# Kernel tuning notes

Measured on AMD Instinct MI355X. Metric: run time of the kernel, lower is better.

The kernel has to match this reference:

```python
import jax, jax.numpy as jnp
import numpy as np

D = 256            # number of graph nodes (example.size(3))
K1 = D // 2        # topkpool1 k
K2 = D // 4        # topkpool2 k
B = 8


def _lrelu(x):
    return jnp.where(x > 0, x, 0.33 * x)


def _e2e(h, wa, ba, wb, bb):
    # h: [B,C,d,d]; wa,wb: [P,C,d] (squeezed (1,d)/(d,1) conv kernels)
    # cnn1: contract over columns j -> [B,P,d]; cnn2: contract over rows i -> [B,P,d]
    a = jnp.einsum('bcij,pcj->bpi', h, wa) + ba[None, :, None]
    b = jnp.einsum('bcij,pci->bpj', h, wb) + bb[None, :, None]
    # cat([a]*d, 3) + cat([b]*d, 2)  ==  broadcast-add
    return a[:, :, :, None] + b[:, :, None, :]


def _gcn(h, g, W, b):
    # h: [B,N,F_in], g: [B,N,N]; faithful to norm_g: g[i,j] / deg[j] (column-normalized
    # because torch broadcasts the [N] degree vector over the LAST dim)
    gb = (g > 0).astype(h.dtype)
    deg = gb.sum(axis=2)                      # [B,N] row sums
    gn = gb / deg[:, None, :]                 # divide column j by deg[j]
    return jnp.einsum('bij,bjf->bif', gn, h) @ W.T + b


def _pool(h, g, s, k):
    # h: [B,N,F], g: [B,N,N], s: [B,N,1] -> top-k nodes by score (descending)
    vals, idx = jax.lax.top_k(s[:, :, 0], k)              # [B,k]
    hn = jnp.take_along_axis(h, idx[:, :, None], axis=1)  # [B,k,F]
    gn = jnp.take_along_axis(g, idx[:, :, None], axis=1)
    gn = jnp.take_along_axis(gn, idx[:, None, :], axis=2) # [B,k,k]
    return hn, gn, vals[:, :, None]


def _readout(h):
    # h: [B,N,F] (node axis = 1); torch ReadOut on [B,F,N,1] max/mean over dim=2
    return jnp.concatenate([h.max(axis=1), h.mean(axis=1)], axis=1)  # [B,2F]


def _forward(x, w1a, b1a, w1b, b1b, w2a, b2a, w2b, b2b, e2n_w, e2n_b,
             a11_w, a11_b, a12_w, a12_b, g1_w, g1_b,
             a21_w, a21_b, a22_w, a22_b,
             d1_w, d1_b, d2_w, d2_b, d3_w, d3_b):
    h = _lrelu(_e2e(x, w1a, b1a, w1b, b1b))         # [B,128,d,d]
    h = _lrelu(_e2e(h, w2a, b2a, w2b, b2b))         # [B,256,d,d]
    # E2N conv (1,d): [B,8,d,1] -> node features [B,d,8]
    nodes = _lrelu(jnp.einsum('bcij,pcj->bpi', h, e2n_w) + e2n_b[None, :, None])
    nodes = jnp.transpose(nodes, (0, 2, 1))          # [B,d,8]
    g0 = x[:, 0]                                     # [B,d,d]

    w = _lrelu(_gcn(nodes, g0, a11_w, a11_b))        # [B,d,1]
    w = jax.nn.sigmoid(_gcn(w, g0, a12_w, a12_b))
    h1, g1, s1 = _pool(nodes, g0, w, K1)             # [B,K1,8], [B,K1,K1], [B,K1,1]
    out = h1 * s1 + h1
    sum1 = _readout(out)                             # [B,16]

    h2 = _gcn(out, g1, g1_w, g1_b)                   # [B,K1,8] (no activation, as in torch)
    w = _lrelu(_gcn(h2, g1, a21_w, a21_b))
    w = jax.nn.sigmoid(_gcn(w, g1, a22_w, a22_b))
    h3, g2, s2 = _pool(h2, g1, w, K2)                # [B,K2,8]
    out2 = h3 * s2 + h3
    sum2 = _readout(out2)                            # [B,16]

    z = sum1 + sum2                                  # [B,16]
    z = _lrelu(z @ d1_w.T + d1_b)                    # dropout = identity (eval mode)
    z = _lrelu(z @ d2_w.T + d2_b)
    return z @ d3_w.T + d3_b                         # [B,1]


def setup_inputs() -> dict:
    key = jax.random.key(0)
    ks = jax.random.split(key, 16)
    f32 = jnp.float32

    def rn(k, shape, scale):
        return jax.random.normal(k, shape, dtype=f32) * scale

    return {
        'x': jax.random.normal(ks[0], (B, 1, D, D), dtype=f32),
        'w1a': rn(ks[1], (128, 1, D), 0.08),  'b1a': jnp.zeros((128,), f32),
        'w1b': rn(ks[2], (128, 1, D), 0.08),  'b1b': jnp.zeros((128,), f32),
        'w2a': rn(ks[3], (256, 128, D), 0.008), 'b2a': jnp.zeros((256,), f32),
        'w2b': rn(ks[4], (256, 128, D), 0.008), 'b2b': jnp.zeros((256,), f32),
        'e2n_w': rn(ks[5], (8, 256, D), 0.005), 'e2n_b': jnp.zeros((8,), f32),
        'a11_w': rn(ks[6], (1, 8), 0.3),  'a11_b': jnp.zeros((1,), f32),
        'a12_w': rn(ks[7], (1, 1), 0.3),  'a12_b': jnp.zeros((1,), f32),
        'g1_w': rn(ks[8], (8, 8), 0.3),   'g1_b': jnp.zeros((8,), f32),
        'a21_w': rn(ks[9], (1, 8), 0.3),  'a21_b': jnp.zeros((1,), f32),
        'a22_w': rn(ks[10], (1, 1), 0.3), 'a22_b': jnp.zeros((1,), f32),
        'd1_w': rn(ks[11], (128, 16), 0.2), 'd1_b': jnp.zeros((128,), f32),
        'd2_w': rn(ks[12], (64, 128), 0.08), 'd2_b': jnp.zeros((64,), f32),
        'd3_w': rn(ks[13], (1, 64), 0.1),  'd3_b': jnp.zeros((1,), f32),
    }


def reference(x, w1a, b1a, w1b, b1b, w2a, b2a, w2b, b2b, e2n_w, e2n_b,
              a11_w, a11_b, a12_w, a12_b, g1_w, g1_b,
              a21_w, a21_b, a22_w, a22_b,
              d1_w, d1_b, d2_w, d2_b, d3_w, d3_b):
    return _forward(x, w1a, b1a, w1b, b1b, w2a, b2a, w2b, b2b, e2n_w, e2n_b,
                    a11_w, a11_b, a12_w, a12_b, g1_w, g1_b,
                    a21_w, a21_b, a22_w, a22_b,
                    d1_w, d1_b, d2_w, d2_b, d3_w, d3_b)
```

## Files before the change

### kernel.cpp

```cpp
#include <hip/hip_runtime.h>

typedef short s16x8 __attribute__((ext_vector_type(8)));
typedef float f32x4 __attribute__((ext_vector_type(4)));
typedef float f32x2 __attribute__((ext_vector_type(2)));

#define TID threadIdx.x

__device__ __forceinline__ float lrelu_f(float x) { return fmaxf(x, 0.33f * x); }

__device__ __forceinline__ unsigned lrelu_pack(float pv, f32x2 q) {
    f32x2 s = q + pv;
    f32x2 m = s * 0.33f;
    f32x2 r = __builtin_elementwise_max(s, m);
    unsigned u;
    asm("v_cvt_pk_bf16_f32 %0, %1, %2" : "=v"(u) : "v"(r.x), "v"(r.y));
    return u;
}
__device__ __forceinline__ unsigned pk_bf16(float a, float b) {
    unsigned u;
    asm("v_cvt_pk_bf16_f32 %0, %1, %2" : "=v"(u) : "v"(a), "v"(b));
    return u;
}

union FragU { s16x8 v; uint4 q; unsigned w[4]; };

__global__ __launch_bounds__(256) void k_convert(
    const float* __restrict__ sa, unsigned short* __restrict__ da, int na4,
    const float* __restrict__ sb, unsigned short* __restrict__ db, int nb4,
    const float* __restrict__ sc, unsigned short* __restrict__ dc, int nc4)
{
    const float* s; unsigned short* d; int n4;
    if (blockIdx.y == 0)      { s = sa; d = da; n4 = na4; }
    else if (blockIdx.y == 1) { s = sb; d = db; n4 = nb4; }
    else                      { s = sc; d = dc; n4 = nc4; }
    const int stride = gridDim.x * 256;
    for (int i = blockIdx.x * 256 + TID; i < n4; i += stride) {
        float4 v = ((const float4*)s)[i];
        ((uint2*)d)[i] = make_uint2(pk_bf16(v.x, v.y), pk_bf16(v.z, v.w));
    }
}

__global__ __launch_bounds__(128) void k_l1(
    const float* __restrict__ x,
    const float* __restrict__ w1a, const float* __restrict__ b1a,
    const float* __restrict__ w1b, const float* __restrict__ b1b,
    float* __restrict__ A1, float* __restrict__ B1)
{
    const int r = blockIdx.x, b = blockIdx.y, v = blockIdx.z;
    const int tid = TID;
    __shared__ float xr[256];
    const float* xb = x + b * 65536;
    if (v == 0) {
        xr[tid]       = xb[r * 256 + tid];
        xr[tid + 128] = xb[r * 256 + tid + 128];
    } else {
        xr[tid]       = xb[tid * 256 + r];
        xr[tid + 128] = xb[(tid + 128) * 256 + r];
    }
    __syncthreads();
    const float* w    = v ? w1b : w1a;
    const float* bias = v ? b1b : b1a;
    float* OUT = v ? B1 : A1;
    float acc = bias[tid];
    const float* wr = w + tid * 256;
    #pragma unroll 4
    for (int q = 0; q < 256; q += 8) {
        float4 a = *(const float4*)(wr + q);
        float4 c = *(const float4*)(wr + q + 4);
        acc += xr[q + 0] * a.x + xr[q + 1] * a.y + xr[q + 2] * a.z + xr[q + 3] * a.w;
        acc += xr[q + 4] * c.x + xr[q + 5] * c.y + xr[q + 6] * c.z + xr[q + 7] * c.w;
    }
    OUT[b * 32768 + tid * 256 + r] = acc;
}

__global__ __launch_bounds__(512) void k_e2e(
    const float* __restrict__ A1, const float* __restrict__ B1,
    const unsigned short* __restrict__ w2aM, const unsigned short* __restrict__ w2bM,
    float* __restrict__ part)
{
    const int rt = blockIdx.x;
    const int s  = blockIdx.y;
    const int bw = blockIdx.z;
    const int b = bw >> 1, which = bw & 1;
    const float* P = (which ? B1 : A1) + b * 32768;
    const float* Q = (which ? A1 : B1) + b * 32768;
    const unsigned short* W = which ? w2bM : w2aM;
    const int c0 = s * 16, r0 = rt * 128;

    __shared__ float Qs[16][256];
    __shared__ float Ps[16][128];

    const int tid = TID;
    {
        const float4* Qg = (const float4*)(Q + c0 * 256);
        float4* Qd = (float4*)&Qs[0][0];
        Qd[tid]       = Qg[tid];
        Qd[tid + 512] = Qg[tid + 512];
        int row = tid >> 5, col = tid & 31;
        *(float4*)&Ps[row][col * 4] = *(const float4*)&P[(c0 + row) * 256 + r0 + col * 4];
    }
    __syncthreads();

    const int wave = tid >> 6, lane = tid & 63, quad = lane >> 4, l16 = lane & 15;
    const int wi = wave & 3, wj = wave >> 2;
    const int pbase = wi * 64, rbase = wj * 64;

    f32x4 acc[4][4] = {};

    const unsigned short* Wrow[4];
    #pragma unroll
    for (int pf = 0; pf < 4; ++pf)
        Wrow[pf] = W + (size_t)(pbase + pf * 16 + l16) * 32768 + c0 * 256 + quad * 8;

    FragU af[2][4];
    f32x2 qp[2][4];
    float pv[4], pvn[4];

    #pragma unroll
    for (int pf = 0; pf < 4; ++pf) af[0][pf].q = *(const uint4*)(Wrow[pf]);
    #pragma unroll
    for (int k = 0; k < 4; ++k) qp[0][k] = *(const f32x2*)&Qs[0][quad * 8 + 2 * k];
    #pragma unroll
    for (int nf = 0; nf < 4; ++nf) pv[nf] = Ps[0][rbase + nf * 16 + l16];

    for (int c = 0; c < 16; ++c) {
        #pragma unroll
        for (int q0 = 0; q0 < 8; ++q0) {
            const int cur = q0 & 1, nxt = cur ^ 1;
            const int cn = (q0 == 7) ? c + 1 : c;
            const int qn = (q0 + 1) & 7;
            if (cn < 16) {
                #pragma unroll
                for (int pf = 0; pf < 4; ++pf)
                    af[nxt][pf].q = *(const uint4*)(Wrow[pf] + cn * 256 + qn * 32);
                #pragma unroll
                for (int k = 0; k < 4; ++k)
                    qp[nxt][k] = *(const f32x2*)&Qs[cn][qn * 32 + quad * 8 + 2 * k];
            }
            if (q0 == 4 && c + 1 < 16) {
                #pragma unroll
                for (int nf = 0; nf < 4; ++nf) pvn[nf] = Ps[c + 1][rbase + nf * 16 + l16];
            }
            #pragma unroll
            for (int nf = 0; nf < 4; ++nf) {
                FragU hb;
                hb.w[0] = lrelu_pack(pv[nf], qp[cur][0]);
                hb.w[1] = lrelu_pack(pv[nf], qp[cur][1]);
                hb.w[2] = lrelu_pack(pv[nf], qp[cur][2]);
                hb.w[3] = lrelu_pack(pv[nf], qp[cur][3]);
                #pragma unroll
                for (int pf = 0; pf < 4; ++pf)
                    acc[pf][nf] = __builtin_amdgcn_mfma_f32_16x16x32_bf16(af[cur][pf].v, hb.v, acc[pf][nf], 0, 0, 0);
            }
            if (q0 == 7) {
                #pragma unroll
                for (int nf = 0; nf < 4; ++nf) pv[nf] = pvn[nf];
            }
        }
    }
    float* pb = part + (size_t)(s * 16 + bw) * 65536;
    #pragma unroll
    for (int pf = 0; pf < 4; ++pf)
        #pragma unroll
        for (int nf = 0; nf < 4; ++nf)
            #pragma unroll
            for (int t = 0; t < 4; ++t) {
                int p = pbase + pf * 16 + quad * 4 + t;
                int r = r0 + rbase + nf * 16 + l16;
                pb[p * 256 + r] = acc[pf][nf][t];
            }
}

__global__ __launch_bounds__(256) void k_red(
    const float* __restrict__ part,
    const float* __restrict__ b2a, const float* __restrict__ b2b,
    float* __restrict__ A2, float* __restrict__ B2)
{
    const int bw = blockIdx.y; const int b = bw >> 1, which = bw & 1;
    const int idx = blockIdx.x * 256 + TID;
    const float4* pp = (const float4*)part;
    float4 acc = make_float4(0.f, 0.f, 0.f, 0.f);
    #pragma unroll
    for (int s = 0; s < 8; ++s) {
        float4 v = pp[(size_t)(s * 16 + bw) * 16384 + idx];
        acc.x += v.x; acc.y += v.y; acc.z += v.z; acc.w += v.w;
    }
    const int p = idx >> 6;
    const float bias = (which ? b2b : b2a)[p];
    acc.x += bias; acc.y += bias; acc.z += bias; acc.w += bias;
    float* OUT = (which ? B2 : A2) + b * 65536;
    ((float4*)OUT)[idx] = acc;
}

__global__ __launch_bounds__(256) void k_e2n(
    const float* __restrict__ A2, const float* __restrict__ B2,
    const unsigned short* __restrict__ e2nw,
    float* __restrict__ nodes_raw)
{
    const int it = blockIdx.x, b = blockIdx.y, sn = blockIdx.z;
    const int tid = TID, wave = tid >> 6, lane = tid & 63, quad = lane >> 4, l16 = lane & 15;
    const int i0 = it * 16;
    const int c0 = sn * 32 + wave * 8;
    const float* Ab = A2 + b * 65536;
    const float* Bb = B2 + b * 65536;
    const float* Brow0 = Bb + c0 * 256 + quad * 8;
    const unsigned short* Wrow0 = e2nw + (size_t)l16 * 65536 + c0 * 256 + quad * 8;

    f32x4 acc = {};
    FragU af[2];
    f32x2 qp[2][4];
    float pv, pvn;

    if (l16 < 8) af[0].q = *(const uint4*)(Wrow0);
    else         af[0].q = make_uint4(0u, 0u, 0u, 0u);
    #pragma unroll
    for (int k = 0; k < 4; ++k) qp[0][k] = *(const f32x2*)(Brow0 + 2 * k);
    pv = Ab[c0 * 256 + i0 + l16];

    for (int cc = 0; cc < 8; ++cc) {
        #pragma unroll
        for (int q0 = 0; q0 < 8; ++q0) {
            const int cur = q0 & 1, nxt = cur ^ 1;
            const int cn = (q0 == 7) ? cc + 1 : cc;
            const int qn = (q0 + 1) & 7;
            if (cn < 8) {
                if (l16 < 8) af[nxt].q = *(const uint4*)(Wrow0 + cn * 256 + qn * 32);
                else         af[nxt].q = make_uint4(0u, 0u, 0u, 0u);
                #pragma unroll
                for (int k = 0; k < 4; ++k)
                    qp[nxt][k] = *(const f32x2*)(Brow0 + cn * 256 + qn * 32 + 2 * k);
            }
            if (q0 == 4 && cc + 1 < 8) pvn = Ab[(c0 + cc + 1) * 256 + i0 + l16];
            FragU hb;
            hb.w[0] = lrelu_pack(pv, qp[cur][0]);
            hb.w[1] = lrelu_pack(pv, qp[cur][1]);
            hb.w[2] = lrelu_pack(pv, qp[cur][2]);
            hb.w[3] = lrelu_pack(pv, qp[cur][3]);
            acc = __builtin_amdgcn_mfma_f32_16x16x32_bf16(af[cur].v, hb.v, acc, 0, 0, 0);
            if (q0 == 7) pv = pvn;
        }
    }
    __shared__ float red[4][16][16];
    #pragma unroll
    for (int t = 0; t < 4; ++t) red[wave][quad * 4 + t][l16] = acc[t];
    __syncthreads();
    const int row = tid >> 4, col = tid & 15;
    if (row < 8) {
        float ssum = red[0][row][col] + red[1][row][col] + red[2][row][col] + red[3][row][col];
        atomicAdd(&nodes_raw[b * 2048 + (i0 + col) * 8 + row], ssum);
    }
}

__global__ __launch_bounds__(256) void k_adj(
    const float* __restrict__ x,
    unsigned long long* __restrict__ adjw, float* __restrict__ rdegw)
{
    const int b = blockIdx.y;
    const int tid = TID, wave = tid >> 6, lane = tid & 63;
    const int rbase = blockIdx.x * 32 + wave * 8;
    for (int rr = 0; rr < 8; ++rr) {
        const int row = rbase + rr;
        int d = 0;
        unsigned long long w[4];
        #pragma unroll
        for (int k = 0; k < 4; ++k) {
            float v = x[b * 65536 + row * 256 + k * 64 + lane];
            w[k] = __ballot(v > 0.0f);
            d += __popcll(w[k]);
        }
        if (lane == 0) {
            #pragma unroll
            for (int k = 0; k < 4; ++k) adjw[(b * 256 + row) * 4 + k] = w[k];
            rdegw[b * 256 + row] = d ? 1.0f / (float)d : 0.0f;
        }
    }
}

__global__ __launch_bounds__(256) void k_tail(
    const unsigned long long* __restrict__ adjw, const float* __restrict__ rdegw,
    const float* __restrict__ nodes_raw, const float* __restrict__ e2n_b,
    const float* __restrict__ a11_w, const float* __restrict__ a11_b,
    const float* __restrict__ a12_w, const float* __restrict__ a12_b,
    const float* __restrict__ g1_w,  const float* __restrict__ g1_b,
    const float* __restrict__ a21_w, const float* __restrict__ a21_b,
    const float* __restrict__ a22_w, const float* __restrict__ a22_b,
    const float* __restrict__ d1_w,  const float* __restrict__ d1_b,
    const float* __restrict__ d2_w,  const float* __restrict__ d2_b,
    const float* __restrict__ d3_w,  const float* __restrict__ d3_b,
    float* __restrict__ out)
{
    const int b = blockIdx.x;
    const int tid = TID;

    __shared__ unsigned long long adj[256][4];
    __shared__ float nod[256][8];
    __shared__ float rdeg[256];
    __shared__ float md[256];
    __shared__ float w1s[256];
    __shared__ float w2s[256];
    __shared__ int   selflag[256];
    __shared__ int   selidx[128];
    __shared__ float s1v[128];
    __shared__ float out1[128][8];
    __shared__ float aggL[128][8];
    __shared__ float h2L[128][8];
    __shared__ unsigned long long adj1[128][2];
    __shared__ float rdeg1[128];
    __shared__ float tA[128];
    __shared__ float w1t[128];
    __shared__ float w2t[128];
    __shared__ int   sel2flag[128];
    __shared__ int   sel2idx[64];
    __shared__ float s2v[64];
    __shared__ float out2[64][8];
    __shared__ float r1[16], r2[16], zz[16];
    __shared__ float z1[128];
    __shared__ float z2[64];

    if (tid < 128) { selidx[tid] = 0; s1v[tid] = 0.0f; }
    if (tid < 64)  { sel2idx[tid] = 0; s2v[tid] = 0.0f; }

    {
        #pragma unroll
        for (int k = 0; k < 4; ++k) adj[tid][k] = adjw[(b * 256 + tid) * 4 + k];
        rdeg[tid] = rdegw[b * 256 + tid];
        for (int f = 0; f < 8; ++f)
            nod[tid][f] = lrelu_f(nodes_raw[b * 2048 + tid * 8 + f] + e2n_b[f]);
    }
    __syncthreads();
    {
        float s = 0.0f;
        for (int f = 0; f < 8; ++f) s += nod[tid][f] * a11_w[f];
        md[tid] = s * rdeg[tid];
    }
    __syncthreads();
    {
        float s = 0.0f;
        for (int k = 0; k < 4; ++k) {
            unsigned long long m = adj[tid][k];
            while (m) { int j = __builtin_ctzll(m); m &= m - 1; s += md[k * 64 + j]; }
        }
        w1s[tid] = lrelu_f(s + a11_b[0]);
    }
    __syncthreads();
    md[tid] = w1s[tid] * a12_w[0] * rdeg[tid];
    __syncthreads();
    {
        float s = 0.0f;
        for (int k = 0; k < 4; ++k) {
            unsigned long long m = adj[tid][k];
            while (m) { int j = __builtin_ctzll(m); m &= m - 1; s += md[k * 64 + j]; }
        }
        w2s[tid] = 1.0f / (1.0f + expf(-(s + a12_b[0])));
    }
    __syncthreads();
    {
        const float my = w2s[tid];
        int cnt = 0;
        for (int j = 0; j < 256; ++j) {
            float o = w2s[j];
            cnt += (o > my) || (o == my && j < tid);
        }
        selflag[tid] = (cnt < 128) ? 1 : 0;
    }
    __syncthreads();
    if (selflag[tid]) {
        int pos = 0;
        for (int j = 0; j < tid; ++j) pos += selflag[j];
        if (pos < 128) { selidx[pos] = tid; s1v[pos] = w2s[tid]; }
    }
    __syncthreads();
    for (int k = tid; k < 1024; k += 256) {
        int t = k >> 3, f = k & 7;
        out1[t][f] = nod[selidx[t]][f] * (1.0f + s1v[t]);
    }
    __syncthreads();
    if (tid < 16) {
        int f = tid & 7;
        if (tid < 8) {
            float mx = -INFINITY;
            for (int t = 0; t < 128; ++t) mx = fmaxf(mx, out1[t][f]);
            r1[tid] = mx;
        } else {
            float s = 0.0f;
            for (int t = 0; t < 128; ++t) s += out1[t][f];
            r1[tid] = s * (1.0f / 128.0f);
        }
    }
    if (tid < 128) {
        unsigned long long wds[2] = {0ull, 0ull};
        const int gi = selidx[tid];
        for (int u = 0; u < 128; ++u) {
            const int gj = selidx[u];
            unsigned long long bit = (adj[gi][gj >> 6] >> (gj & 63)) & 1ull;
            wds[u >> 6] |= bit << (u & 63);
        }
        adj1[tid][0] = wds[0]; adj1[tid][1] = wds[1];
        int d = __popcll(wds[0]) + __popcll(wds[1]);
        rdeg1[tid] = d ? 1.0f / (float)d : 0.0f;
    }
    __syncthreads();
    {
        const int t = tid >> 1, f0 = (tid & 1) * 4;
        float a0 = 0, a1 = 0, a2 = 0, a3 = 0;
        for (int k = 0; k < 2; ++k) {
            unsigned long long m = adj1[t][k];
            while (m) {
                int u = __builtin_ctzll(m); m &= m - 1;
                int uu = k * 64 + u;
                float rr = rdeg1[uu];
                a0 += out1[uu][f0 + 0] * rr;
                a1 += out1[uu][f0 + 1] * rr;
                a2 += out1[uu][f0 + 2] * rr;
                a3 += out1[uu][f0 + 3] * rr;
            }
        }
        aggL[t][f0 + 0] = a0; aggL[t][f0 + 1] = a1; aggL[t][f0 + 2] = a2; aggL[t][f0 + 3] = a3;
    }
    __syncthreads();
    for (int k = tid; k < 1024; k += 256) {
        int t = k >> 3, fo = k & 7;
        float s = g1_b[fo];
        for (int f = 0; f < 8; ++f) s += aggL[t][f] * g1_w[fo * 8 + f];
        h2L[t][fo] = s;
    }
    __syncthreads();
    if (tid < 128) {
        float s = 0.0f;
        for (int f = 0; f < 8; ++f) s += h2L[tid][f] * a21_w[f];
        tA[tid] = s * rdeg1[tid];
    }
    __syncthreads();
    if (tid < 128) {
        float s = 0.0f;
        for (int k = 0; k < 2; ++k) {
            unsigned long long m = adj1[tid][k];
            while (m) { int u = __builtin_ctzll(m); m &= m - 1; s += tA[k * 64 + u]; }
        }
        w1t[tid] = lrelu_f(s + a21_b[0]);
    }
    __syncthreads();
    if (tid < 128) tA[tid] = w1t[tid] * a22_w[0] * rdeg1[tid];
    __syncthreads();
    if (tid < 128) {
        float s = 0.0f;
        for (int k = 0; k < 2; ++k) {
            unsigned long long m = adj1[tid][k];
            while (m) { int u = __builtin_ctzll(m); m &= m - 1; s += tA[k * 64 + u]; }
        }
        w2t[tid] = 1.0f / (1.0f + expf(-(s + a22_b[0])));
    }
    __syncthreads();
    if (tid < 128) {
        const float my = w2t[tid];
        int cnt = 0;
        for (int u = 0; u < 128; ++u) {
            float o = w2t[u];
            cnt += (o > my) || (o == my && u < tid);
        }
        sel2flag[tid] = (cnt < 64) ? 1 : 0;
    }
    __syncthreads();
    if (tid < 128 && sel2flag[tid]) {
        int pos = 0;
        for (int u = 0; u < tid; ++u) pos += sel2flag[u];
        if (pos < 64) { sel2idx[pos] = tid; s2v[pos] = w2t[tid]; }
    }
    __syncthreads();
    for (int k = tid; k < 512; k += 256) {
        int u = k >> 3, f = k & 7;
        out2[u][f] = h2L[sel2idx[u]][f] * (1.0f + s2v[u]);
    }
    __syncthreads();
    if (tid < 16) {
        int f = tid & 7;
        if (tid < 8) {
            float mx = -INFINITY;
            for (int t = 0; t < 64; ++t) mx = fmaxf(mx, out2[t][f]);
            r2[tid] = mx;
        } else {
            float s = 0.0f;
            for (int t = 0; t < 64; ++t) s += out2[t][f];
            r2[tid] = s * (1.0f / 64.0f);
        }
    }
    __syncthreads();
    if (tid < 16) zz[tid] = r1[tid] + r2[tid];
    __syncthreads();
    if (tid < 128) {
        float s = d1_b[tid];
        for (int k = 0; k < 16; ++k) s += zz[k] * d1_w[tid * 16 + k];
        z1[tid] = lrelu_f(s);
    }
    __syncthreads();
    if (tid < 64) {
        float s = d2_b[tid];
        for (int k = 0; k < 128; ++k) s += z1[k] * d2_w[tid * 128 + k];
        z2[tid] = lrelu_f(s);
    }
    __syncthreads();
    if (tid == 0) {
        float s = d3_b[0];
        for (int k = 0; k < 64; ++k) s += z2[k] * d3_w[k];
        out[b] = s;
    }
}

extern "C" void kernel_launch(void* const* d_in, const int* in_sizes, int n_in,
                              void* d_out, int out_size, void* d_ws, size_t ws_size,
                              hipStream_t stream) {
    const float* x     = (const float*)d_in[0];
    const float* w1a   = (const float*)d_in[1];
    const float* b1a   = (const float*)d_in[2];
    const float* w1b   = (const float*)d_in[3];
    const float* b1b   = (const float*)d_in[4];
    const float* w2a   = (const float*)d_in[5];
    const float* b2a   = (const float*)d_in[6];
    const float* w2b   = (const float*)d_in[7];
    const float* b2b   = (const float*)d_in[8];
    const float* e2nw  = (const float*)d_in[9];

    float* ws        = (float*)d_ws;
    float* A1        = ws;
    float* B1        = ws + 262144;
    float* A2        = ws + 524288;
    float* B2        = ws + 1048576;
    float* nodes_raw = ws + 1572864;
    float* rdegw     = ws + 1589248;
    unsigned long long* adjw = (unsigned long long*)(ws + 1597440);
    float* part      = ws + 1613824;
    unsigned short* w2aM  = (unsigned short*)(ws + 10002432);
    unsigned short* w2bM  = w2aM + 8388608;
    unsigned short* e2nwM = w2bM + 8388608;

    k_convert<<<dim3(512, 3), 256, 0, stream>>>(
        w2a, w2aM, 8388608 / 4,
        w2b, w2bM, 8388608 / 4,
        e2nw, e2nwM, 524288 / 4);
    hipMemsetAsync(nodes_raw, 0, 16384 * sizeof(float), stream);
    k_l1<<<dim3(256, 8, 2), 128, 0, stream>>>(x, w1a, b1a, w1b, b1b, A1, B1);
    k_adj<<<dim3(8, 8), 256, 0, stream>>>(x, adjw, rdegw);
    k_e2e<<<dim3(2, 8, 16), 512, 0, stream>>>(A1, B1, w2aM, w2bM, part);
    k_red<<<dim3(64, 16), 256, 0, stream>>>(part, b2a, b2b, A2, B2);
    k_e2n<<<dim3(16, 8, 8), 256, 0, stream>>>(A2, B2, e2nwM, nodes_raw);
    k_tail<<<dim3(8), 256, 0, stream>>>(adjw, rdegw, nodes_raw, (const float*)d_in[10],
        (const float*)d_in[11], (const float*)d_in[12], (const float*)d_in[13], (const float*)d_in[14],
        (const float*)d_in[15], (const float*)d_in[16], (const float*)d_in[17], (const float*)d_in[18],
        (const float*)d_in[19], (const float*)d_in[20], (const float*)d_in[21], (const float*)d_in[22],
        (const float*)d_in[23], (const float*)d_in[24], (const float*)d_in[25], (const float*)d_in[26],
        (float*)d_out);
}
```

Before: 439.4 us.

## Precompute lrelu-packed bf16 B fragments cooperatively in double-buffered LDS

After: 442.3 us. Within noise of the previous version (+0.7%).

```diff
diff --git a/kernel.cpp b/kernel.cpp
--- a/kernel.cpp
+++ b/kernel.cpp
@@ -89,8 +89,14 @@
 
     __shared__ float Qs[16][256];
     __shared__ float Ps[16][128];
+    __shared__ uint4 Hs[2][4096];
 
     const int tid = TID;
+    const int wave = tid >> 6, lane = tid & 63, quad = lane >> 4, l16 = lane & 15;
+    const int wi = wave & 3, wj = wave >> 2;
+    const int pbase = wi * 64, rbase = wj * 64;
+    const int hbase = wj * 4;
+
     {
         const float4* Qg = (const float4*)(Q + c0 * 256);
         float4* Qd = (float4*)&Qs[0][0];
@@ -101,9 +107,24 @@
     }
     __syncthreads();
 
-    const int wave = tid >> 6, lane = tid & 63, quad = lane >> 4, l16 = lane & 15;
-    const int wi = wave & 3, wj = wave >> 2;
-    const int pbase = wi * 64, rbase = wj * 64;
+    {
+        const int qb = wave * 32 + quad * 8;
+        f32x2 q0p = *(const f32x2*)&Qs[0][qb + 0];
+        f32x2 q1p = *(const f32x2*)&Qs[0][qb + 2];
+        f32x2 q2p = *(const f32x2*)&Qs[0][qb + 4];
+        f32x2 q3p = *(const f32x2*)&Qs[0][qb + 6];
+        #pragma unroll
+        for (int rf = 0; rf < 8; ++rf) {
+            float pv = Ps[0][rf * 16 + l16];
+            uint4 u;
+            u.x = lrelu_pack(pv, q0p);
+            u.y = lrelu_pack(pv, q1p);
+            u.z = lrelu_pack(pv, q2p);
+            u.w = lrelu_pack(pv, q3p);
+            Hs[0][(wave * 8 + rf) * 64 + lane] = u;
+        }
+    }
+    __syncthreads();
 
     f32x4 acc[4][4] = {};
 
@@ -113,51 +134,60 @@
         Wrow[pf] = W + (size_t)(pbase + pf * 16 + l16) * 32768 + c0 * 256 + quad * 8;
 
     FragU af[2][4];
-    f32x2 qp[2][4];
-    float pv[4], pvn[4];
-
     #pragma unroll
     for (int pf = 0; pf < 4; ++pf) af[0][pf].q = *(const uint4*)(Wrow[pf]);
-    #pragma unroll
-    for (int k = 0; k < 4; ++k) qp[0][k] = *(const f32x2*)&Qs[0][quad * 8 + 2 * k];
-    #pragma unroll
-    for (int nf = 0; nf < 4; ++nf) pv[nf] = Ps[0][rbase + nf * 16 + l16];
 
     for (int c = 0; c < 16; ++c) {
+        const int cb = c & 1, nb = cb ^ 1;
+
+        f32x2 q0p, q1p, q2p, q3p;
+        if (c + 1 < 16) {
+            const int qb = wave * 32 + quad * 8;
+            q0p = *(const f32x2*)&Qs[c + 1][qb + 0];
+            q1p = *(const f32x2*)&Qs[c + 1][qb + 2];
+            q2p = *(const f32x2*)&Qs[c + 1][qb + 4];
+            q3p = *(const f32x2*)&Qs[c + 1][qb + 6];
+        }
+
+        FragU hbf[2][4];
+        #pragma unroll
+        for (int nf = 0; nf < 4; ++nf)
+            hbf[0][nf].q = Hs[cb][(hbase + nf) * 64 + lane];
+
         #pragma unroll
         for (int q0 = 0; q0 < 8; ++q0) {
             const int cur = q0 & 1, nxt = cur ^ 1;
+
             const int cn = (q0 == 7) ? c + 1 : c;
             const int qn = (q0 + 1) & 7;
             if (cn < 16) {
                 #pragma unroll
                 for (int pf = 0; pf < 4; ++pf)
                     af[nxt][pf].q = *(const uint4*)(Wrow[pf] + cn * 256 + qn * 32);
+            }
+            if (q0 < 7) {
                 #pragma unroll
-                for (int k = 0; k < 4; ++k)
-                    qp[nxt][k] = *(const f32x2*)&Qs[cn][qn * 32 + quad * 8 + 2 * k];
+                for (int nf = 0; nf < 4; ++nf)
+                    hbf[nxt][nf].q = Hs[cb][((q0 + 1) * 8 + hbase + nf) * 64 + lane];
             }
-            if (q0 == 4 && c + 1 < 16) {
-                #pragma unroll
-                for (int nf = 0; nf < 4; ++nf) pvn[nf] = Ps[c + 1][rbase + nf * 16 + l16];
+            if (c + 1 < 16) {
+                float pv = Ps[c + 1][q0 * 16 + l16];
+                uint4 u;
+                u.x = lrelu_pack(pv, q0p);
+                u.y = lrelu_pack(pv, q1p);
+                u.z = lrelu_pack(pv, q2p);
+                u.w = lrelu_pack(pv, q3p);
+                Hs[nb][(wave * 8 + q0) * 64 + lane] = u;
             }
             #pragma unroll
-            for (int nf = 0; nf < 4; ++nf) {
-                FragU hb;
-                hb.w[0] = lrelu_pack(pv[nf], qp[cur][0]);
-                hb.w[1] = lrelu_pack(pv[nf], qp[cur][1]);
-                hb.w[2] = lrelu_pack(pv[nf], qp[cur][2]);
-                hb.w[3] = lrelu_pack(pv[nf], qp[cur][3]);
+            for (int nf = 0; nf < 4; ++nf)
                 #pragma unroll
                 for (int pf = 0; pf < 4; ++pf)
-                    acc[pf][nf] = __builtin_amdgcn_mfma_f32_16x16x32_bf16(af[cur][pf].v, hb.v, acc[pf][nf], 0, 0, 0);
-            }
-            if (q0 == 7) {
-                #pragma unroll
-                for (int nf = 0; nf < 4; ++nf) pv[nf] = pvn[nf];
-            }
-        }
-    }
+                    acc[pf][nf] = __builtin_amdgcn_mfma_f32_16x16x32_bf16(af[cur][pf].v, hbf[cur][nf].v, acc[pf][nf], 0, 0, 0);
+        }
+        __syncthreads();
+    }
+
     float* pb = part + (size_t)(s * 16 + bw) * 65536;
     #pragma unroll
     for (int pf = 0; pf < 4; ++pf)
```

## Stage E2E weight tiles through LDS with XCD-aware block mapping

Applied to the files above, without the earlier changes.

New measurement: 607.9 us. 1.38x slower.

```diff
diff --git a/kernel.cpp b/kernel.cpp
--- a/kernel.cpp
+++ b/kernel.cpp
@@ -73,101 +73,106 @@
     OUT[b * 32768 + tid * 256 + r] = acc;
 }
 
-__global__ __launch_bounds__(512) void k_e2e(
+__global__ __launch_bounds__(256) void k_e2e(
     const float* __restrict__ A1, const float* __restrict__ B1,
     const unsigned short* __restrict__ w2aM, const unsigned short* __restrict__ w2bM,
     float* __restrict__ part)
 {
-    const int rt = blockIdx.x;
-    const int s  = blockIdx.y;
-    const int bw = blockIdx.z;
-    const int b = bw >> 1, which = bw & 1;
+    const int bid = blockIdx.x;
+    const int xcd = bid & 7, tt = bid >> 3;
+    const int hi = tt >> 5, inner = tt & 31;
+    const int slice = xcd + 8 * hi;
+    const int s = slice >> 1, which = slice & 1;
+    const int rt = inner >> 3, b = inner & 7;
+    const int bw = b * 2 + which;
+
     const float* P = (which ? B1 : A1) + b * 32768;
     const float* Q = (which ? A1 : B1) + b * 32768;
     const unsigned short* W = which ? w2bM : w2aM;
-    const int c0 = s * 16, r0 = rt * 128;
+    const int c0 = s * 16, r0 = rt * 64;
 
     __shared__ float Qs[16][256];
-    __shared__ float Ps[16][128];
+    __shared__ float Ps[16][64];
+    __shared__ uint4 Wl[1024];
 
     const int tid = TID;
+    const int wave = tid >> 6, lane = tid & 63, quad = lane >> 4, l16 = lane & 15;
+
     {
         const float4* Qg = (const float4*)(Q + c0 * 256);
         float4* Qd = (float4*)&Qs[0][0];
-        Qd[tid]       = Qg[tid];
-        Qd[tid + 512] = Qg[tid + 512];
-        int row = tid >> 5, col = tid & 31;
-        *(float4*)&Ps[row][col * 4] = *(const float4*)&P[(c0 + row) * 256 + r0 + col * 4];
-    }
-    __syncthreads();
-
-    const int wave = tid >> 6, lane = tid & 63, quad = lane >> 4, l16 = lane & 15;
-    const int wi = wave & 3, wj = wave >> 2;
-    const int pbase = wi * 64, rbase = wj * 64;
+        #pragma unroll
+        for (int u = 0; u < 4; ++u) Qd[tid + u * 256] = Qg[tid + u * 256];
+        const int prow = tid >> 4, pc4 = (tid & 15) * 4;
+        *(float4*)&Ps[prow][pc4] = *(const float4*)&P[(c0 + prow) * 256 + r0 + pc4];
+    }
+
+    const int wrow = tid >> 2, wcol = tid & 3;
+    const unsigned short* Wg = W + (size_t)wrow * 32768 + c0 * 256 + wcol * 8;
+
+    uint4 wreg[4];
+    #pragma unroll
+    for (int u = 0; u < 4; ++u)
+        wreg[u] = *(const uint4*)(Wg + (size_t)u * 64 * 32768);
+
+    __syncthreads();
 
     f32x4 acc[4][4] = {};
 
-    const unsigned short* Wrow[4];
-    #pragma unroll
-    for (int pf = 0; pf < 4; ++pf)
-        Wrow[pf] = W + (size_t)(pbase + pf * 16 + l16) * 32768 + c0 * 256 + quad * 8;
-
-    FragU af[2][4];
-    f32x2 qp[2][4];
-    float pv[4], pvn[4];
-
-    #pragma unroll
-    for (int pf = 0; pf < 4; ++pf) af[0][pf].q = *(const uint4*)(Wrow[pf]);
-    #pragma unroll
-    for (int k = 0; k < 4; ++k) qp[0][k] = *(const f32x2*)&Qs[0][quad * 8 + 2 * k];
-    #pragma unroll
-    for (int nf = 0; nf < 4; ++nf) pv[nf] = Ps[0][rbase + nf * 16 + l16];
-
-    for (int c = 0; c < 16; ++c) {
-        #pragma unroll
-        for (int q0 = 0; q0 < 8; ++q0) {
-            const int cur = q0 & 1, nxt = cur ^ 1;
-            const int cn = (q0 == 7) ? c + 1 : c;
-            const int qn = (q0 + 1) & 7;
-            if (cn < 16) {
-                #pragma unroll
-                for (int pf = 0; pf < 4; ++pf)
-                    af[nxt][pf].q = *(const uint4*)(Wrow[pf] + cn * 256 + qn * 32);
-                #pragma unroll
-                for (int k = 0; k < 4; ++k)
-                    qp[nxt][k] = *(const f32x2*)&Qs[cn][qn * 32 + quad * 8 + 2 * k];
-            }
-            if (q0 == 4 && c + 1 < 16) {
-                #pragma unroll
-                for (int nf = 0; nf < 4; ++nf) pvn[nf] = Ps[c + 1][rbase + nf * 16 + l16];
-            }
+    for (int t = 0; t < 128; ++t) {
+        #pragma unroll
+        for (int u = 0; u < 4; ++u)
+            Wl[(u * 64 + wrow) * 4 + wcol] = wreg[u];
+        __syncthreads();
+
+        if (t + 1 < 128) {
+            const int cn = (t + 1) >> 3, qn = (t + 1) & 7;
+            const unsigned short* src = Wg + cn * 256 + qn * 32;
             #pragma unroll
-            for (int nf = 0; nf < 4; ++nf) {
-                FragU hb;
-                hb.w[0] = lrelu_pack(pv[nf], qp[cur][0]);
-                hb.w[1] = lrelu_pack(pv[nf], qp[cur][1]);
-                hb.w[2] = lrelu_pack(pv[nf], qp[cur][2]);
-                hb.w[3] = lrelu_pack(pv[nf], qp[cur][3]);
-                #pragma unroll
-                for (int pf = 0; pf < 4; ++pf)
-                    acc[pf][nf] = __builtin_amdgcn_mfma_f32_16x16x32_bf16(af[cur][pf].v, hb.v, acc[pf][nf], 0, 0, 0);
-            }
-            if (q0 == 7) {
-                #pragma unroll
-                for (int nf = 0; nf < 4; ++nf) pv[nf] = pvn[nf];
-            }
-        }
-    }
+            for (int u = 0; u < 4; ++u)
+                wreg[u] = *(const uint4*)(src + (size_t)u * 64 * 32768);
+        }
+
+        const int c = t >> 3, qc = t & 7;
+
+        FragU af[4];
+        #pragma unroll
+        for (int pf = 0; pf < 4; ++pf)
+            af[pf].q = Wl[(wave * 64 + pf * 16 + l16) * 4 + quad];
+
+        f32x2 qp[4];
+        #pragma unroll
+        for (int m = 0; m < 4; ++m)
+            qp[m] = *(const f32x2*)&Qs[c][qc * 32 + quad * 8 + 2 * m];
+        FragU hb[4];
+        #pragma unroll
+        for (int nf = 0; nf < 4; ++nf) {
+            const float pv = Ps[c][nf * 16 + l16];
+            hb[nf].w[0] = lrelu_pack(pv, qp[0]);
+            hb[nf].w[1] = lrelu_pack(pv, qp[1]);
+            hb[nf].w[2] = lrelu_pack(pv, qp[2]);
+            hb[nf].w[3] = lrelu_pack(pv, qp[3]);
+        }
+
+        #pragma unroll
+        for (int nf = 0; nf < 4; ++nf)
+            #pragma unroll
+            for (int pf = 0; pf < 4; ++pf)
+                acc[pf][nf] = __builtin_amdgcn_mfma_f32_16x16x32_bf16(af[pf].v, hb[nf].v, acc[pf][nf], 0, 0, 0);
+
+        __syncthreads();
+    }
+
     float* pb = part + (size_t)(s * 16 + bw) * 65536;
     #pragma unroll
     for (int pf = 0; pf < 4; ++pf)
         #pragma unroll
         for (int nf = 0; nf < 4; ++nf)
             #pragma unroll
-            for (int t = 0; t < 4; ++t) {
-                int p = pbase + pf * 16 + quad * 4 + t;
-                int r = r0 + rbase + nf * 16 + l16;
-                pb[p * 256 + r] = acc[pf][nf][t];
+            for (int e = 0; e < 4; ++e) {
+                int p = wave * 64 + pf * 16 + quad * 4 + e;
+                int r = r0 + nf * 16 + l16;
+                pb[p * 256 + r] = acc[pf][nf][e];
             }
 }
 
@@ -540,7 +545,7 @@
     hipMemsetAsync(nodes_raw, 0, 16384 * sizeof(float), stream);
     k_l1<<<dim3(256, 8, 2), 128, 0, stream>>>(x, w1a, b1a, w1b, b1b, A1, B1);
     k_adj<<<dim3(8, 8), 256, 0, stream>>>(x, adjw, rdegw);
-    k_e2e<<<dim3(2, 8, 16), 512, 0, stream>>>(A1, B1, w2aM, w2bM, part);
+    k_e2e<<<dim3(512), 256, 0, stream>>>(A1, B1, w2aM, w2bM, part);
     k_red<<<dim3(64, 16), 256, 0, stream>>>(part, b2a, b2b, A2, B2);
     k_e2n<<<dim3(16, 8, 8), 256, 0, stream>>>(A2, B2, e2nwM, nodes_raw);
     k_tail<<<dim3(8), 256, 0, stream>>>(adjw, rdegw, nodes_raw, (const float*)d_in[10],
```
